# Performance work log

Measured on AMD Instinct MI355X. Metric: run time of the kernel, lower is better.

Reference implementation:

```python
import jax, jax.numpy as jnp
import numpy as np
import math

D_MODEL = 768
B, S = 8, 2048


def setup_inputs() -> dict:
    key = jax.random.key(0)
    k1, k2, k3, k4, k5 = jax.random.split(key, 5)
    return {
        "input": jax.random.normal(k1, (B, S, D_MODEL), dtype=jnp.float32),
        "attention_mask": jax.random.randint(k2, (B,), 0, S + 1, dtype=jnp.int32),
        "Wq": jax.random.normal(k3, (D_MODEL, D_MODEL), dtype=jnp.float32),
        "Wk": jax.random.normal(k4, (D_MODEL, D_MODEL), dtype=jnp.float32),
        "Wv": jax.random.normal(k5, (D_MODEL, D_MODEL), dtype=jnp.float32),
    }


def reference(input, attention_mask, Wq, Wk, Wv):
    d_model = Wq.shape[0]
    # QKV projections (v is computed in the original but never used in the output)
    q = jnp.matmul(input, Wq)  # [B,S,D]
    k = jnp.matmul(input, Wk)  # [B,S,D]
    v = jnp.matmul(input, Wv)  # [B,S,D] (dead in original forward output)
    # Per-sample QK^T, vectorized instead of the original python loop+cat
    attention_score = jnp.einsum("bqd,bkd->bqk", q, k) / math.sqrt(float(d_model) ** 3)
    # Ragged mask: positions (j,k) with j<len_i and k<len_i keep the score, else -1000.
    # Built with vectorized arange comparisons instead of the original triple python loop.
    idx = jnp.arange(attention_score.shape[1])  # [S]
    valid = idx[None, :] < attention_mask[:, None]  # [B,S]
    keep = valid[:, :, None] & valid[:, None, :]  # [B,S,S]
    mask_attention_score = jnp.where(keep, attention_score, jnp.float32(-1000.0))
    attention_score_n = jax.nn.softmax(mask_attention_score, axis=-1)  # computed but unused, as in original
    # Original returns UNMASKED, pre-softmax scores matmul'd with the raw input (not v).
    self_attention = jnp.einsum("bqk,bkd->bqd", attention_score, input)
    return self_attention
```

## Files before the change

kernel.cpp:

```cpp
#include <hip/hip_runtime.h>
#include <hip/hip_bf16.h>
#include <cmath>


typedef __attribute__((ext_vector_type(8))) short short8;
typedef __attribute__((ext_vector_type(4))) float f32x4;

__device__ __forceinline__ unsigned short f2bf(float f) {
    union { float f; unsigned int u; } v; v.f = f;
    unsigned int u = v.u;
    return (unsigned short)((u + 0x7FFFu + ((u >> 16) & 1u)) >> 16);
}

__global__ __launch_bounds__(256)
void convert_w(const float* __restrict__ Wq, const float* __restrict__ Wk,
               unsigned short* __restrict__ Wq16, unsigned short* __restrict__ Wk16)
{
    int i = (blockIdx.x * 256 + threadIdx.x) * 8;
    float4 a = *reinterpret_cast<const float4*>(&Wq[i]);
    float4 b = *reinterpret_cast<const float4*>(&Wq[i + 4]);
    uint4 v;
    v.x = (unsigned)f2bf(a.x) | ((unsigned)f2bf(a.y) << 16);
    v.y = (unsigned)f2bf(a.z) | ((unsigned)f2bf(a.w) << 16);
    v.z = (unsigned)f2bf(b.x) | ((unsigned)f2bf(b.y) << 16);
    v.w = (unsigned)f2bf(b.z) | ((unsigned)f2bf(b.w) << 16);
    *reinterpret_cast<uint4*>(&Wq16[i]) = v;
    a = *reinterpret_cast<const float4*>(&Wk[i]);
    b = *reinterpret_cast<const float4*>(&Wk[i + 4]);
    v.x = (unsigned)f2bf(a.x) | ((unsigned)f2bf(a.y) << 16);
    v.y = (unsigned)f2bf(a.z) | ((unsigned)f2bf(a.w) << 16);
    v.z = (unsigned)f2bf(b.x) | ((unsigned)f2bf(b.y) << 16);
    v.w = (unsigned)f2bf(b.z) | ((unsigned)f2bf(b.w) << 16);
    *reinterpret_cast<uint4*>(&Wk16[i]) = v;
}

__global__ __launch_bounds__(256)
void transpose_bf16(const float* __restrict__ X, unsigned short* __restrict__ Xt,
                    unsigned short* __restrict__ Xbf, int S, int D)
{
    __shared__ unsigned short tile[32][36];
    const int b = blockIdx.z;
    const int s0 = blockIdx.x * 32;
    const int d0 = blockIdx.y * 32;
    const float* Xb = X + (size_t)b * S * D;
    unsigned short* Xtb = Xt + (size_t)b * S * D;
    unsigned short* Xbb = Xbf + (size_t)b * S * D;
    const int tx = threadIdx.x & 7;
    const int ty = threadIdx.x >> 3;

    float4 v = *reinterpret_cast<const float4*>(&Xb[(size_t)(s0 + ty) * D + d0 + tx * 4]);
    ushort4 pk;
    pk.x = f2bf(v.x); pk.y = f2bf(v.y); pk.z = f2bf(v.z); pk.w = f2bf(v.w);
    *reinterpret_cast<ushort4*>(&Xbb[(size_t)(s0 + ty) * D + d0 + tx * 4]) = pk;
    tile[tx * 4 + 0][ty] = pk.x;
    tile[tx * 4 + 1][ty] = pk.y;
    tile[tx * 4 + 2][ty] = pk.z;
    tile[tx * 4 + 3][ty] = pk.w;
    __syncthreads();
    ushort4 o;
    o.x = tile[ty][tx * 4 + 0];
    o.y = tile[ty][tx * 4 + 1];
    o.z = tile[ty][tx * 4 + 2];
    o.w = tile[ty][tx * 4 + 3];
    *reinterpret_cast<ushort4*>(&Xtb[(size_t)(d0 + ty) * S + s0 + tx * 4]) = o;
}

template <int ROWS>
__device__ __forceinline__ void stage_glds(const unsigned short* src, unsigned short* lds,
                                           int ld, int tid)
{
    #pragma unroll
    for (int it = 0; it < ROWS / 32; ++it) {
        int slot = it * 256 + tid;
        int r = slot >> 3, c = slot & 7;
        const unsigned short* gp = src + (size_t)r * ld + ((c ^ (r & 7)) << 3);
        unsigned short* lp = lds + (size_t)(it * 256 + (tid & 192)) * 8;
        __builtin_amdgcn_global_load_lds(
            (__attribute__((address_space(1))) void*)(void*)gp,
            (__attribute__((address_space(3))) void*)lp, 16, 0, 0);
    }
}

__device__ __forceinline__ void store_c(float* C, size_t i, float v) { C[i] = v; }
__device__ __forceinline__ void store_c(unsigned short* C, size_t i, float v) { C[i] = f2bf(v); }

template <int TM, int TN, typename CT>
__global__ __launch_bounds__(256)
void gemm(const unsigned short* __restrict__ Ap, const unsigned short* __restrict__ Bp,
          CT* __restrict__ Cb,
          int Kloop, int lda, int ldb, int ldc, long sA, long sB, long sC, float alpha)
{
    constexpr int FM = TM / 32;
    constexpr int FN = TN / 32;
    const int b = blockIdx.x;
    CT* C = Cb + (long)b * sC;

    __shared__ unsigned short Alds[TM * 64];
    __shared__ unsigned short Blds[TN * 64];

    const int tid  = threadIdx.x;
    const int lane = tid & 63;
    const int wave = tid >> 6;
    const int wr   = (wave >> 1) * (TM / 2);
    const int wc   = (wave & 1) * (TN / 2);
    const int rowBase = blockIdx.y * TM;
    const int colBase = blockIdx.z * TN;
    const int l15  = lane & 15;
    const int quad = lane >> 4;

    f32x4 acc[FM][FN] = {};

    for (int k0 = 0; k0 < Kloop; k0 += 64) {
        stage_glds<TM>(Ap + (long)b * sA + (size_t)rowBase * lda + k0, Alds, lda, tid);
        stage_glds<TN>(Bp + (long)b * sB + (size_t)colBase * ldb + k0, Blds, ldb, tid);
        __syncthreads();

        short8 af[FM][2], bfr[FN][2];
        #pragma unroll
        for (int i = 0; i < FM; ++i) {
            int ra = wr + i * 16 + l15;
            af[i][0] = *reinterpret_cast<const short8*>(&Alds[ra * 64 + ((quad ^ (ra & 7)) << 3)]);
            af[i][1] = *reinterpret_cast<const short8*>(&Alds[ra * 64 + (((quad + 4) ^ (ra & 7)) << 3)]);
        }
        #pragma unroll
        for (int i = 0; i < FN; ++i) {
            int rb = wc + i * 16 + l15;
            bfr[i][0] = *reinterpret_cast<const short8*>(&Blds[rb * 64 + ((quad ^ (rb & 7)) << 3)]);
            bfr[i][1] = *reinterpret_cast<const short8*>(&Blds[rb * 64 + (((quad + 4) ^ (rb & 7)) << 3)]);
        }
        #pragma unroll
        for (int ks = 0; ks < 2; ++ks)
            #pragma unroll
            for (int mi = 0; mi < FM; ++mi)
                #pragma unroll
                for (int ni = 0; ni < FN; ++ni)
                    acc[mi][ni] = __builtin_amdgcn_mfma_f32_16x16x32_bf16(
                        af[mi][ks], bfr[ni][ks], acc[mi][ni], 0, 0, 0);
        __syncthreads();
    }

    #pragma unroll
    for (int mi = 0; mi < FM; ++mi) {
        #pragma unroll
        for (int ni = 0; ni < FN; ++ni) {
            int col = colBase + wc + ni * 16 + l15;
            #pragma unroll
            for (int r = 0; r < 4; ++r) {
                int row = rowBase + wr + mi * 16 + quad * 4 + r;
                store_c(C, (size_t)row * ldc + col, alpha * acc[mi][ni][r]);
            }
        }
    }
}

extern "C" void kernel_launch(void* const* d_in, const int* in_sizes, int n_in,
                              void* d_out, int out_size, void* d_ws, size_t ws_size,
                              hipStream_t stream)
{
    const float* X  = (const float*)d_in[0];
    const float* Wq = (const float*)d_in[2];
    const float* Wk = (const float*)d_in[3];
    float* out = (float*)d_out;

    const int Bn = 8, S = 2048, D = 768;
    const float alpha = 1.0f / (768.0f * sqrtf(768.0f));
    const size_t szX  = (size_t)Bn * S * D;
    const size_t szDD = (size_t)Bn * D * D;

    unsigned short* Xt16 = (unsigned short*)d_ws;
    unsigned short* Xbf  = Xt16 + szX;
    unsigned short* P16  = Xbf + szX;
    unsigned short* G16  = P16 + (size_t)D * D;
    unsigned short* Ht16 = G16 + szDD;
    unsigned short* Wq16 = Ht16 + szDD;
    unsigned short* Wk16 = Wq16 + (size_t)D * D;

    convert_w<<<dim3(D * D / 2048, 1, 1), 256, 0, stream>>>(Wq, Wk, Wq16, Wk16);

    transpose_bf16<<<dim3(S / 32, D / 32, Bn), 256, 0, stream>>>(X, Xt16, Xbf, S, D);

    gemm<64, 64, unsigned short><<<dim3(1, 12, 12), 256, 0, stream>>>(
        Wq16, Wk16, P16, D, D, D, D, 0L, 0L, 0L, 1.0f);

    gemm<96, 96, unsigned short><<<dim3(Bn, 8, 8), 256, 0, stream>>>(
        Xt16, Xt16, G16, S, S, S, D, (long)D * S, (long)D * S, (long)D * D, 1.0f);

    gemm<96, 96, unsigned short><<<dim3(Bn, 8, 8), 256, 0, stream>>>(
        G16, P16, Ht16, D, D, D, D, (long)D * D, 0L, (long)D * D, alpha);

    gemm<128, 128, float><<<dim3(Bn, S / 128, 6), 256, 0, stream>>>(
        Xbf, Ht16, out, D, D, D, D, (long)S * D, (long)D * D, (long)S * D, 1.0f);
}
```

Baseline: 193.6 us.

## Double-buffer GEMM LDS staging and exploit symmetry of the Gram matrix

The GEMM kernel gets two LDS buffers, so the next K tile is prefetched with global_load_lds while MFMAs run on the current one. The X^T X Gram GEMM now computes only upper-triangle tiles and writes each off-diagonal tile to both positions, roughly halving its work. The costs are double the LDS footprint, which may lower occupancy for the 96 and 128 tiles, and strided mirrored stores. One barrier per iteration remains, and a wait on the async loads is needed before reading the prefetched buffer, so this relies on ordering that may be fragile.

```diff
diff --git a/kernel.cpp b/kernel.cpp
--- a/kernel.cpp
+++ b/kernel.cpp
@@ -84,7 +84,7 @@
 __device__ __forceinline__ void store_c(float* C, size_t i, float v) { C[i] = v; }
 __device__ __forceinline__ void store_c(unsigned short* C, size_t i, float v) { C[i] = f2bf(v); }
 
-template <int TM, int TN, typename CT>
+template <int TM, int TN, bool SYMM, typename CT>
 __global__ __launch_bounds__(256)
 void gemm(const unsigned short* __restrict__ Ap, const unsigned short* __restrict__ Bp,
           CT* __restrict__ Cb,
@@ -92,11 +92,12 @@
 {
     constexpr int FM = TM / 32;
     constexpr int FN = TN / 32;
+    if (SYMM && blockIdx.y > blockIdx.z) return;
     const int b = blockIdx.x;
     CT* C = Cb + (long)b * sC;
 
-    __shared__ unsigned short Alds[TM * 64];
-    __shared__ unsigned short Blds[TN * 64];
+    __shared__ unsigned short Alds[2][TM * 64];
+    __shared__ unsigned short Blds[2][TN * 64];
 
     const int tid  = threadIdx.x;
     const int lane = tid & 63;
@@ -108,25 +109,35 @@
     const int l15  = lane & 15;
     const int quad = lane >> 4;
 
+    const unsigned short* Abase = Ap + (long)b * sA + (size_t)rowBase * lda;
+    const unsigned short* Bbase = Bp + (long)b * sB + (size_t)colBase * ldb;
+
     f32x4 acc[FM][FN] = {};
 
-    for (int k0 = 0; k0 < Kloop; k0 += 64) {
-        stage_glds<TM>(Ap + (long)b * sA + (size_t)rowBase * lda + k0, Alds, lda, tid);
-        stage_glds<TN>(Bp + (long)b * sB + (size_t)colBase * ldb + k0, Blds, ldb, tid);
-        __syncthreads();
+    stage_glds<TM>(Abase, &Alds[0][0], lda, tid);
+    stage_glds<TN>(Bbase, &Blds[0][0], ldb, tid);
+    __syncthreads();
+
+    const int nt = Kloop >> 6;
+    for (int t = 0; t < nt; ++t) {
+        const int cur = t & 1;
+        if (t + 1 < nt) {
+            stage_glds<TM>(Abase + (t + 1) * 64, &Alds[cur ^ 1][0], lda, tid);
+            stage_glds<TN>(Bbase + (t + 1) * 64, &Blds[cur ^ 1][0], ldb, tid);
+        }
 
         short8 af[FM][2], bfr[FN][2];
         #pragma unroll
         for (int i = 0; i < FM; ++i) {
             int ra = wr + i * 16 + l15;
-            af[i][0] = *reinterpret_cast<const short8*>(&Alds[ra * 64 + ((quad ^ (ra & 7)) << 3)]);
-            af[i][1] = *reinterpret_cast<const short8*>(&Alds[ra * 64 + (((quad + 4) ^ (ra & 7)) << 3)]);
+            af[i][0] = *reinterpret_cast<const short8*>(&Alds[cur][ra * 64 + ((quad ^ (ra & 7)) << 3)]);
+            af[i][1] = *reinterpret_cast<const short8*>(&Alds[cur][ra * 64 + (((quad + 4) ^ (ra & 7)) << 3)]);
         }
         #pragma unroll
         for (int i = 0; i < FN; ++i) {
             int rb = wc + i * 16 + l15;
-            bfr[i][0] = *reinterpret_cast<const short8*>(&Blds[rb * 64 + ((quad ^ (rb & 7)) << 3)]);
-            bfr[i][1] = *reinterpret_cast<const short8*>(&Blds[rb * 64 + (((quad + 4) ^ (rb & 7)) << 3)]);
+            bfr[i][0] = *reinterpret_cast<const short8*>(&Blds[cur][rb * 64 + ((quad ^ (rb & 7)) << 3)]);
+            bfr[i][1] = *reinterpret_cast<const short8*>(&Blds[cur][rb * 64 + (((quad + 4) ^ (rb & 7)) << 3)]);
         }
         #pragma unroll
         for (int ks = 0; ks < 2; ++ks)
@@ -136,6 +147,7 @@
                 for (int ni = 0; ni < FN; ++ni)
                     acc[mi][ni] = __builtin_amdgcn_mfma_f32_16x16x32_bf16(
                         af[mi][ks], bfr[ni][ks], acc[mi][ni], 0, 0, 0);
+
         __syncthreads();
     }
 
@@ -149,6 +161,17 @@
                 int row = rowBase + wr + mi * 16 + quad * 4 + r;
                 store_c(C, (size_t)row * ldc + col, alpha * acc[mi][ni][r]);
             }
+            if constexpr (SYMM) {
+                if (blockIdx.y < blockIdx.z) {
+                    ushort4 m;
+                    m.x = f2bf(alpha * acc[mi][ni][0]);
+                    m.y = f2bf(alpha * acc[mi][ni][1]);
+                    m.z = f2bf(alpha * acc[mi][ni][2]);
+                    m.w = f2bf(alpha * acc[mi][ni][3]);
+                    size_t mbase = (size_t)col * ldc + rowBase + wr + mi * 16 + quad * 4;
+                    *reinterpret_cast<ushort4*>(&((unsigned short*)C)[mbase]) = m;
+                }
+            }
         }
     }
 }
@@ -179,15 +202,15 @@
 
     transpose_bf16<<<dim3(S / 32, D / 32, Bn), 256, 0, stream>>>(X, Xt16, Xbf, S, D);
 
-    gemm<64, 64, unsigned short><<<dim3(1, 12, 12), 256, 0, stream>>>(
+    gemm<64, 64, false, unsigned short><<<dim3(1, 12, 12), 256, 0, stream>>>(
         Wq16, Wk16, P16, D, D, D, D, 0L, 0L, 0L, 1.0f);
 
-    gemm<96, 96, unsigned short><<<dim3(Bn, 8, 8), 256, 0, stream>>>(
+    gemm<96, 96, true, unsigned short><<<dim3(Bn, 8, 8), 256, 0, stream>>>(
         Xt16, Xt16, G16, S, S, S, D, (long)D * S, (long)D * S, (long)D * D, 1.0f);
 
-    gemm<96, 96, unsigned short><<<dim3(Bn, 8, 8), 256, 0, stream>>>(
+    gemm<96, 96, false, unsigned short><<<dim3(Bn, 8, 8), 256, 0, stream>>>(
         G16, P16, Ht16, D, D, D, D, (long)D * D, 0L, (long)D * D, alpha);
 
-    gemm<128, 128, float><<<dim3(Bn, S / 128, 6), 256, 0, stream>>>(
+    gemm<128, 128, false, float><<<dim3(Bn, S / 128, 6), 256, 0, stream>>>(
         Xbf, Ht16, out, D, D, D, D, (long)S * D, (long)D * D, (long)S * D, 1.0f);
 }
```

After: 197.4 us. About the same (+2.0%).

## Fuse all stages into one persistent kernel with global atomic barriers

Applied to the files above, without the earlier changes.

Replaces the separate convert, transpose and four GEMM launches with a single persistent 256-block kernel. Stages are sequenced by a grid-wide barrier and per-batch spin barriers. The weight bf16 conversion is folded into the P GEMM's LDS staging, and the GEMM main loop gains LDS double buffering. This removes launch gaps and intermediate weight buffers. The cost is less parallelism per stage, and the design relies on all blocks being co-resident for the spin barriers.

```diff
diff --git a/kernel.cpp b/kernel.cpp
--- a/kernel.cpp
+++ b/kernel.cpp
@@ -1,5 +1,4 @@
 #include <hip/hip_runtime.h>
-#include <hip/hip_bf16.h>
 #include <cmath>
 
 
@@ -12,57 +11,26 @@
     return (unsigned short)((u + 0x7FFFu + ((u >> 16) & 1u)) >> 16);
 }
 
-__global__ __launch_bounds__(256)
-void convert_w(const float* __restrict__ Wq, const float* __restrict__ Wk,
-               unsigned short* __restrict__ Wq16, unsigned short* __restrict__ Wk16)
-{
-    int i = (blockIdx.x * 256 + threadIdx.x) * 8;
-    float4 a = *reinterpret_cast<const float4*>(&Wq[i]);
-    float4 b = *reinterpret_cast<const float4*>(&Wq[i + 4]);
-    uint4 v;
-    v.x = (unsigned)f2bf(a.x) | ((unsigned)f2bf(a.y) << 16);
-    v.y = (unsigned)f2bf(a.z) | ((unsigned)f2bf(a.w) << 16);
-    v.z = (unsigned)f2bf(b.x) | ((unsigned)f2bf(b.y) << 16);
-    v.w = (unsigned)f2bf(b.z) | ((unsigned)f2bf(b.w) << 16);
-    *reinterpret_cast<uint4*>(&Wq16[i]) = v;
-    a = *reinterpret_cast<const float4*>(&Wk[i]);
-    b = *reinterpret_cast<const float4*>(&Wk[i + 4]);
-    v.x = (unsigned)f2bf(a.x) | ((unsigned)f2bf(a.y) << 16);
-    v.y = (unsigned)f2bf(a.z) | ((unsigned)f2bf(a.w) << 16);
-    v.z = (unsigned)f2bf(b.x) | ((unsigned)f2bf(b.y) << 16);
-    v.w = (unsigned)f2bf(b.z) | ((unsigned)f2bf(b.w) << 16);
-    *reinterpret_cast<uint4*>(&Wk16[i]) = v;
-}
-
-__global__ __launch_bounds__(256)
-void transpose_bf16(const float* __restrict__ X, unsigned short* __restrict__ Xt,
-                    unsigned short* __restrict__ Xbf, int S, int D)
-{
-    __shared__ unsigned short tile[32][36];
-    const int b = blockIdx.z;
-    const int s0 = blockIdx.x * 32;
-    const int d0 = blockIdx.y * 32;
-    const float* Xb = X + (size_t)b * S * D;
-    unsigned short* Xtb = Xt + (size_t)b * S * D;
-    unsigned short* Xbb = Xbf + (size_t)b * S * D;
-    const int tx = threadIdx.x & 7;
-    const int ty = threadIdx.x >> 3;
-
-    float4 v = *reinterpret_cast<const float4*>(&Xb[(size_t)(s0 + ty) * D + d0 + tx * 4]);
-    ushort4 pk;
-    pk.x = f2bf(v.x); pk.y = f2bf(v.y); pk.z = f2bf(v.z); pk.w = f2bf(v.w);
-    *reinterpret_cast<ushort4*>(&Xbb[(size_t)(s0 + ty) * D + d0 + tx * 4]) = pk;
-    tile[tx * 4 + 0][ty] = pk.x;
-    tile[tx * 4 + 1][ty] = pk.y;
-    tile[tx * 4 + 2][ty] = pk.z;
-    tile[tx * 4 + 3][ty] = pk.w;
-    __syncthreads();
-    ushort4 o;
-    o.x = tile[ty][tx * 4 + 0];
-    o.y = tile[ty][tx * 4 + 1];
-    o.z = tile[ty][tx * 4 + 2];
-    o.w = tile[ty][tx * 4 + 3];
-    *reinterpret_cast<ushort4*>(&Xtb[(size_t)(d0 + ty) * S + s0 + tx * 4]) = o;
+__device__ unsigned g_gbar[64];
+__device__ unsigned g_tbar[8][64];
+
+__device__ __forceinline__ void abarrier(unsigned* cnt, unsigned* gen, unsigned n)
+{
+    __syncthreads();
+    if (threadIdx.x == 0) {
+        __threadfence();
+        unsigned g = __hip_atomic_load(gen, __ATOMIC_RELAXED, __HIP_MEMORY_SCOPE_AGENT);
+        unsigned c = __hip_atomic_fetch_add(cnt, 1u, __ATOMIC_ACQ_REL, __HIP_MEMORY_SCOPE_AGENT);
+        if (c == n - 1u) {
+            __hip_atomic_store(cnt, 0u, __ATOMIC_RELAXED, __HIP_MEMORY_SCOPE_AGENT);
+            __hip_atomic_store(gen, g + 1u, __ATOMIC_RELEASE, __HIP_MEMORY_SCOPE_AGENT);
+        } else {
+            while (__hip_atomic_load(gen, __ATOMIC_RELAXED, __HIP_MEMORY_SCOPE_AGENT) == g)
+                __builtin_amdgcn_s_sleep(2);
+        }
+        __threadfence();
+    }
+    __syncthreads();
 }
 
 template <int ROWS>
@@ -81,52 +49,65 @@
     }
 }
 
+template <int ROWS>
+__device__ __forceinline__ void stage_f32(const float* __restrict__ src, unsigned short* lds,
+                                          int ld, int tid)
+{
+    #pragma unroll
+    for (int it = 0; it < ROWS / 32; ++it) {
+        int slot = it * 256 + tid;
+        int r = slot >> 3, c = slot & 7;
+        const float* gp = src + (size_t)r * ld + c * 8;
+        float4 a = *reinterpret_cast<const float4*>(gp);
+        float4 d = *reinterpret_cast<const float4*>(gp + 4);
+        union { short8 s; unsigned short u[8]; } v;
+        v.u[0] = f2bf(a.x); v.u[1] = f2bf(a.y); v.u[2] = f2bf(a.z); v.u[3] = f2bf(a.w);
+        v.u[4] = f2bf(d.x); v.u[5] = f2bf(d.y); v.u[6] = f2bf(d.z); v.u[7] = f2bf(d.w);
+        *reinterpret_cast<short8*>(&lds[r * 64 + ((c ^ (r & 7)) << 3)]) = v.s;
+    }
+}
+
 __device__ __forceinline__ void store_c(float* C, size_t i, float v) { C[i] = v; }
 __device__ __forceinline__ void store_c(unsigned short* C, size_t i, float v) { C[i] = f2bf(v); }
 
 template <int TM, int TN, typename CT>
-__global__ __launch_bounds__(256)
-void gemm(const unsigned short* __restrict__ Ap, const unsigned short* __restrict__ Bp,
-          CT* __restrict__ Cb,
-          int Kloop, int lda, int ldb, int ldc, long sA, long sB, long sC, float alpha)
-{
-    constexpr int FM = TM / 32;
-    constexpr int FN = TN / 32;
-    const int b = blockIdx.x;
-    CT* C = Cb + (long)b * sC;
-
-    __shared__ unsigned short Alds[TM * 64];
-    __shared__ unsigned short Blds[TN * 64];
-
-    const int tid  = threadIdx.x;
-    const int lane = tid & 63;
-    const int wave = tid >> 6;
-    const int wr   = (wave >> 1) * (TM / 2);
-    const int wc   = (wave & 1) * (TN / 2);
-    const int rowBase = blockIdx.y * TM;
-    const int colBase = blockIdx.z * TN;
-    const int l15  = lane & 15;
-    const int quad = lane >> 4;
+__device__ void gemm_tile(const unsigned short* __restrict__ A0,
+                          const unsigned short* __restrict__ B0,
+                          CT* __restrict__ C, int rowBase, int colBase,
+                          int K, int lda, int ldb, int ldc, float alpha,
+                          unsigned short* lds)
+{
+    constexpr int FM = TM / 32, FN = TN / 32;
+    const int tid = threadIdx.x, lane = tid & 63, wave = tid >> 6;
+    const int wr = (wave >> 1) * (TM / 2), wc = (wave & 1) * (TN / 2);
+    const int l15 = lane & 15, quad = lane >> 4;
+    unsigned short* Al[2] = { lds,           lds + (TM + TN) * 64 };
+    unsigned short* Bl[2] = { lds + TM * 64, lds + (TM + TN) * 64 + TM * 64 };
 
     f32x4 acc[FM][FN] = {};
-
-    for (int k0 = 0; k0 < Kloop; k0 += 64) {
-        stage_glds<TM>(Ap + (long)b * sA + (size_t)rowBase * lda + k0, Alds, lda, tid);
-        stage_glds<TN>(Bp + (long)b * sB + (size_t)colBase * ldb + k0, Blds, ldb, tid);
-        __syncthreads();
-
+    stage_glds<TM>(A0, Al[0], lda, tid);
+    stage_glds<TN>(B0, Bl[0], ldb, tid);
+    __syncthreads();
+
+    const int nt = K >> 6;
+    for (int t = 0; t < nt; ++t) {
+        const int cur = t & 1;
+        if (t + 1 < nt) {
+            stage_glds<TM>(A0 + (t + 1) * 64, Al[cur ^ 1], lda, tid);
+            stage_glds<TN>(B0 + (t + 1) * 64, Bl[cur ^ 1], ldb, tid);
+        }
         short8 af[FM][2], bfr[FN][2];
         #pragma unroll
         for (int i = 0; i < FM; ++i) {
             int ra = wr + i * 16 + l15;
-            af[i][0] = *reinterpret_cast<const short8*>(&Alds[ra * 64 + ((quad ^ (ra & 7)) << 3)]);
-            af[i][1] = *reinterpret_cast<const short8*>(&Alds[ra * 64 + (((quad + 4) ^ (ra & 7)) << 3)]);
+            af[i][0] = *reinterpret_cast<const short8*>(&Al[cur][ra * 64 + ((quad ^ (ra & 7)) << 3)]);
+            af[i][1] = *reinterpret_cast<const short8*>(&Al[cur][ra * 64 + (((quad + 4) ^ (ra & 7)) << 3)]);
         }
         #pragma unroll
         for (int i = 0; i < FN; ++i) {
             int rb = wc + i * 16 + l15;
-            bfr[i][0] = *reinterpret_cast<const short8*>(&Blds[rb * 64 + ((quad ^ (rb & 7)) << 3)]);
-            bfr[i][1] = *reinterpret_cast<const short8*>(&Blds[rb * 64 + (((quad + 4) ^ (rb & 7)) << 3)]);
+            bfr[i][0] = *reinterpret_cast<const short8*>(&Bl[cur][rb * 64 + ((quad ^ (rb & 7)) << 3)]);
+            bfr[i][1] = *reinterpret_cast<const short8*>(&Bl[cur][rb * 64 + (((quad + 4) ^ (rb & 7)) << 3)]);
         }
         #pragma unroll
         for (int ks = 0; ks < 2; ++ks)
@@ -140,7 +121,7 @@
     }
 
     #pragma unroll
-    for (int mi = 0; mi < FM; ++mi) {
+    for (int mi = 0; mi < FM; ++mi)
         #pragma unroll
         for (int ni = 0; ni < FN; ++ni) {
             int col = colBase + wc + ni * 16 + l15;
@@ -150,6 +131,136 @@
                 store_c(C, (size_t)row * ldc + col, alpha * acc[mi][ni][r]);
             }
         }
+}
+
+__device__ void ptile(const float* __restrict__ Wq, const float* __restrict__ Wk,
+                      unsigned short* __restrict__ P, int ty, int tz,
+                      unsigned short* lds)
+{
+    unsigned short* Al = lds;
+    unsigned short* Bl = lds + 96 * 64;
+    const int tid = threadIdx.x, lane = tid & 63, wave = tid >> 6;
+    const int wr = (wave >> 1) * 48, wc = (wave & 1) * 48;
+    const int l15 = lane & 15, quad = lane >> 4;
+    f32x4 acc[3][3] = {};
+
+    for (int k0 = 0; k0 < 768; k0 += 64) {
+        stage_f32<96>(Wq + (size_t)(ty * 96) * 768 + k0, Al, 768, tid);
+        stage_f32<96>(Wk + (size_t)(tz * 96) * 768 + k0, Bl, 768, tid);
+        __syncthreads();
+        short8 af[3][2], bfr[3][2];
+        #pragma unroll
+        for (int i = 0; i < 3; ++i) {
+            int ra = wr + i * 16 + l15;
+            af[i][0] = *reinterpret_cast<const short8*>(&Al[ra * 64 + ((quad ^ (ra & 7)) << 3)]);
+            af[i][1] = *reinterpret_cast<const short8*>(&Al[ra * 64 + (((quad + 4) ^ (ra & 7)) << 3)]);
+        }
+        #pragma unroll
+        for (int i = 0; i < 3; ++i) {
+            int rb = wc + i * 16 + l15;
+            bfr[i][0] = *reinterpret_cast<const short8*>(&Bl[rb * 64 + ((quad ^ (rb & 7)) << 3)]);
+            bfr[i][1] = *reinterpret_cast<const short8*>(&Bl[rb * 64 + (((quad + 4) ^ (rb & 7)) << 3)]);
+        }
+        #pragma unroll
+        for (int ks = 0; ks < 2; ++ks)
+            #pragma unroll
+            for (int mi = 0; mi < 3; ++mi)
+                #pragma unroll
+                for (int ni = 0; ni < 3; ++ni)
+                    acc[mi][ni] = __builtin_amdgcn_mfma_f32_16x16x32_bf16(
+                        af[mi][ks], bfr[ni][ks], acc[mi][ni], 0, 0, 0);
+        __syncthreads();
+    }
+    #pragma unroll
+    for (int mi = 0; mi < 3; ++mi)
+        #pragma unroll
+        for (int ni = 0; ni < 3; ++ni) {
+            int col = tz * 96 + wc + ni * 16 + l15;
+            #pragma unroll
+            for (int r = 0; r < 4; ++r) {
+                int row = ty * 96 + wr + mi * 16 + quad * 4 + r;
+                P[(size_t)row * 768 + col] = f2bf(acc[mi][ni][r]);
+            }
+        }
+}
+
+__device__ void transp_tile(const float* __restrict__ X, unsigned short* __restrict__ Xt,
+                            unsigned short* __restrict__ Xbf, int bb, int s0, int d0,
+                            unsigned short* tbuf )
+{
+    const float* Xb = X + (size_t)bb * 2048 * 768;
+    unsigned short* Xtb = Xt + (size_t)bb * 2048 * 768;
+    unsigned short* Xbb = Xbf + (size_t)bb * 2048 * 768;
+    const int tx = threadIdx.x & 7, ty = threadIdx.x >> 3;
+
+    float4 v = *reinterpret_cast<const float4*>(&Xb[(size_t)(s0 + ty) * 768 + d0 + tx * 4]);
+    ushort4 pk;
+    pk.x = f2bf(v.x); pk.y = f2bf(v.y); pk.z = f2bf(v.z); pk.w = f2bf(v.w);
+    *reinterpret_cast<ushort4*>(&Xbb[(size_t)(s0 + ty) * 768 + d0 + tx * 4]) = pk;
+    tbuf[(tx * 4 + 0) * 36 + ty] = pk.x;
+    tbuf[(tx * 4 + 1) * 36 + ty] = pk.y;
+    tbuf[(tx * 4 + 2) * 36 + ty] = pk.z;
+    tbuf[(tx * 4 + 3) * 36 + ty] = pk.w;
+    __syncthreads();
+    ushort4 o;
+    o.x = tbuf[ty * 36 + tx * 4 + 0];
+    o.y = tbuf[ty * 36 + tx * 4 + 1];
+    o.z = tbuf[ty * 36 + tx * 4 + 2];
+    o.w = tbuf[ty * 36 + tx * 4 + 3];
+    *reinterpret_cast<ushort4*>(&Xtb[(size_t)(d0 + ty) * 2048 + s0 + tx * 4]) = o;
+    __syncthreads();
+}
+
+__global__ __launch_bounds__(256, 1)
+void mega(const float* __restrict__ X, const float* __restrict__ Wq,
+          const float* __restrict__ Wk, float* __restrict__ out,
+          unsigned short* __restrict__ Xt, unsigned short* __restrict__ Xbf,
+          unsigned short* __restrict__ P16, unsigned short* __restrict__ G16,
+          unsigned short* __restrict__ Ht16, float alpha)
+{
+    __shared__ unsigned short lds[32768];
+    const int r  = blockIdx.x;
+    const int b  = r & 7;
+    const int lr = r >> 3;
+    const int tid = threadIdx.x;
+
+    if (lr < 8) ptile(Wq, Wk, P16, lr, b, lds);
+    {
+        int cnt   = (lr < 8) ? 42 : 50;
+        int start = (lr < 8) ? lr * 42 : 336 + (lr - 8) * 50;
+        for (int i = 0; i < cnt; ++i) {
+            int t = start + i;
+            transp_tile(X, Xt, Xbf, b, (t & 63) * 32, (t >> 6) * 32, lds);
+        }
+    }
+    abarrier(&g_gbar[0], &g_gbar[16], 256);
+
+    const unsigned short* Xtb = Xt + (size_t)b * 768 * 2048;
+    unsigned short* Gb = G16 + (size_t)b * 768 * 768;
+    for (int u = lr; u < 64; u += 32) {
+        int ty = u >> 3, tz = u & 7;
+        gemm_tile<96, 96, unsigned short>(
+            Xtb + (size_t)ty * 96 * 2048, Xtb + (size_t)tz * 96 * 2048,
+            Gb, ty * 96, tz * 96, 2048, 2048, 2048, 768, 1.0f, lds);
+    }
+    abarrier(&g_tbar[b][0], &g_tbar[b][16], 32);
+
+    unsigned short* Htb = Ht16 + (size_t)b * 768 * 768;
+    for (int u = lr; u < 64; u += 32) {
+        int ty = u >> 3, tz = u & 7;
+        gemm_tile<96, 96, unsigned short>(
+            Gb + (size_t)ty * 96 * 768, P16 + (size_t)tz * 96 * 768,
+            Htb, ty * 96, tz * 96, 768, 768, 768, 768, alpha, lds);
+    }
+    abarrier(&g_tbar[b][0], &g_tbar[b][16], 32);
+
+    const unsigned short* Xbb = Xbf + (size_t)b * 2048 * 768;
+    float* outb = out + (size_t)b * 2048 * 768;
+    for (int u = lr; u < 96; u += 32) {
+        int ty = u / 6, tz = u % 6;
+        gemm_tile<128, 128, float>(
+            Xbb + (size_t)ty * 128 * 768, Htb + (size_t)tz * 128 * 768,
+            outb, ty * 128, tz * 128, 768, 768, 768, 768, 1.0f, lds);
     }
 }
 
@@ -172,22 +283,7 @@
     unsigned short* P16  = Xbf + szX;
     unsigned short* G16  = P16 + (size_t)D * D;
     unsigned short* Ht16 = G16 + szDD;
-    unsigned short* Wq16 = Ht16 + szDD;
-    unsigned short* Wk16 = Wq16 + (size_t)D * D;
-
-    convert_w<<<dim3(D * D / 2048, 1, 1), 256, 0, stream>>>(Wq, Wk, Wq16, Wk16);
-
-    transpose_bf16<<<dim3(S / 32, D / 32, Bn), 256, 0, stream>>>(X, Xt16, Xbf, S, D);
-
-    gemm<64, 64, unsigned short><<<dim3(1, 12, 12), 256, 0, stream>>>(
-        Wq16, Wk16, P16, D, D, D, D, 0L, 0L, 0L, 1.0f);
-
-    gemm<96, 96, unsigned short><<<dim3(Bn, 8, 8), 256, 0, stream>>>(
-        Xt16, Xt16, G16, S, S, S, D, (long)D * S, (long)D * S, (long)D * D, 1.0f);
-
-    gemm<96, 96, unsigned short><<<dim3(Bn, 8, 8), 256, 0, stream>>>(
-        G16, P16, Ht16, D, D, D, D, (long)D * D, 0L, (long)D * D, alpha);
-
-    gemm<128, 128, float><<<dim3(Bn, S / 128, 6), 256, 0, stream>>>(
-        Xbf, Ht16, out, D, D, D, D, (long)S * D, (long)D * D, (long)S * D, 1.0f);
-}
+
+    mega<<<dim3(256), dim3(256), 0, stream>>>(X, Wq, Wk, out,
+                                              Xt16, Xbf, P16, G16, Ht16, alpha);
+}
```

Result: slower. 327.0 us (+68.9%).
